# Kernel optimization log

Hardware: AMD Instinct MI355X
Metric: run time of the kernel (lower is better)

## Reference

```python
import jax, jax.numpy as jnp
import numpy as np

N = 50000
E = 800000
IN_DIM = 128
HID = 32
HEADS = 8
OUT_DIM = 64
BN_EPS = 1e-5
NEG_SLOPE = 0.2


def batch_norm(x, gamma, beta, mean, var):
    # eval-mode BatchNorm1d using running statistics
    return (x - mean) * jax.lax.rsqrt(var + BN_EPS) * gamma + beta


def gat_conv(x, src, dst, W, att_src, att_dst, heads, out_ch, n):
    """PyG GATConv (shared src/dst lin), self-loops already included in src/dst.
    x: [n, in]; W: [in, heads*out_ch]; att_*: [heads, out_ch].
    Returns [n, heads, out_ch]."""
    h = (x @ W).reshape(n, heads, out_ch)                       # node features per head
    a_s = jnp.einsum('nho,ho->nh', h, att_src)                  # [n, heads]
    a_d = jnp.einsum('nho,ho->nh', h, att_dst)
    e = jax.nn.leaky_relu(a_s[src] + a_d[dst], NEG_SLOPE)       # [e, heads]
    # segment softmax over incoming edges of each dst node
    mx = jax.ops.segment_max(e, dst, num_segments=n)
    ex = jnp.exp(e - mx[dst])
    denom = jax.ops.segment_sum(ex, dst, num_segments=n)
    alpha = ex / (denom[dst] + 1e-16)                           # [e, heads]
    out = jax.ops.segment_sum(alpha[:, :, None] * h[src], dst, num_segments=n)
    return out                                                  # [n, heads, out_ch]


def setup_inputs() -> dict:
    key = jax.random.key(0)
    ks = jax.random.split(key, 24)
    inp = {}
    inp['x'] = jax.random.normal(ks[0], (N, IN_DIM), dtype=jnp.float32)
    inp['edge_index'] = jax.random.randint(ks[1], (2, E), 0, N, dtype=jnp.int64)
    s = 0.05
    inp['W1'] = jax.random.normal(ks[2], (IN_DIM, HEADS * HID), dtype=jnp.float32) * s
    inp['a_src1'] = jax.random.normal(ks[3], (HEADS, HID), dtype=jnp.float32) * s
    inp['a_dst1'] = jax.random.normal(ks[4], (HEADS, HID), dtype=jnp.float32) * s
    inp['b1'] = jnp.zeros((HEADS * HID,), dtype=jnp.float32)
    inp['W2'] = jax.random.normal(ks[5], (HEADS * HID, OUT_DIM), dtype=jnp.float32) * s
    inp['a_src2'] = jax.random.normal(ks[6], (1, OUT_DIM), dtype=jnp.float32) * s
    inp['a_dst2'] = jax.random.normal(ks[7], (1, OUT_DIM), dtype=jnp.float32) * s
    inp['b2'] = jnp.zeros((OUT_DIM,), dtype=jnp.float32)
    # projection Linear(out_dim -> in_dim)
    inp['Wp'] = jax.random.normal(ks[8], (OUT_DIM, IN_DIM), dtype=jnp.float32) * s
    inp['bp'] = jnp.zeros((IN_DIM,), dtype=jnp.float32)
    # BatchNorm params (eval mode running stats)
    for i, d in [(1, HEADS * HID), (2, OUT_DIM), (3, IN_DIM)]:
        k0, k1, k2, k3 = jax.random.split(ks[8 + i], 4)
        inp[f'g{i}'] = 1.0 + 0.1 * jax.random.normal(k0, (d,), dtype=jnp.float32)
        inp[f'be{i}'] = 0.1 * jax.random.normal(k1, (d,), dtype=jnp.float32)
        inp[f'm{i}'] = 0.1 * jax.random.normal(k2, (d,), dtype=jnp.float32)
        inp[f'v{i}'] = jax.random.uniform(k3, (d,), dtype=jnp.float32, minval=0.5, maxval=1.5)
    return inp


def reference(x, edge_index, W1, a_src1, a_dst1, b1, W2, a_src2, a_dst2, b2,
              Wp, bp, g1, be1, m1, v1, g2, be2, m2, v2, g3, be3, m3, v3):
    n = x.shape[0]
    loops = jnp.arange(n, dtype=edge_index.dtype)
    src = jnp.concatenate([edge_index[0], loops])   # add_self_loops=True (PyG default)
    dst = jnp.concatenate([edge_index[1], loops])

    h = gat_conv(x, src, dst, W1, a_src1, a_dst1, HEADS, HID, n)
    h = h.reshape(n, HEADS * HID) + b1              # concat=True
    h = jax.nn.elu(batch_norm(h, g1, be1, m1, v1))  # dropout is no-op in eval

    h = gat_conv(h, src, dst, W2, a_src2, a_dst2, 1, OUT_DIM, n)
    h = h.reshape(n, OUT_DIM) + b2                  # concat=False, heads=1 -> mean == identity
    h = jax.nn.elu(batch_norm(h, g2, be2, m2, v2))

    h = h @ Wp + bp
    return batch_norm(h, g3, be3, m3, v3)
```

## Files before the change

### kernel.cpp

```cpp
#include <hip/hip_runtime.h>
#include <math.h>

#define NEG_SLOPE 0.2f
#define BN_EPS 1e-5f

typedef __bf16 bf16x8 __attribute__((ext_vector_type(8)));
typedef float  f32x4  __attribute__((ext_vector_type(4)));

__device__ __forceinline__ float elu_f(float x){ return x > 0.f ? x : expm1f(x); }
__device__ __forceinline__ float lrelu_f(float x){ return x > 0.f ? x : NEG_SLOPE * x; }

__device__ __forceinline__ float b2f(ushort u){
    union { uint i; float f; } v; v.i = (uint)u << 16; return v.f;
}
__device__ __forceinline__ ushort f2b(float f){
    union { float f; uint i; } v; v.f = f;
    uint r = v.i + 0x7FFFu + ((v.i >> 16) & 1u);
    return (ushort)(r >> 16);
}

__global__ void setup_kernel(const void* ei, int n_check, long long N, int* flag64,
    const float* __restrict__ W1, const float* __restrict__ W2, const float* __restrict__ Wp,
    ushort* __restrict__ wt1, ushort* __restrict__ wt2, ushort* __restrict__ wtp,
    const float* b1, const float* b2, const float* bp,
    const float* g1, const float* be1, const float* m1, const float* v1,
    const float* g2, const float* be2, const float* m2, const float* v2,
    const float* g3, const float* be3, const float* m3, const float* v3,
    float* par)
{
    int b = blockIdx.x, t = threadIdx.x;
    if (b == 0) {
        __shared__ int oks;
        if (t == 0) oks = 1;
        __syncthreads();
        const long long* p = (const long long*)ei;
        int ok = 1;
        for (int i = t; i < n_check; i += 256) {
            long long v = p[i];
            if (v < 0 || v >= N) ok = 0;
        }
        if (!ok) oks = 0;
        __syncthreads();
        if (t == 0) *flag64 = oks;
        { float s = g1[t] * rsqrtf(v1[t] + BN_EPS); par[t] = s;        par[256 + t] = b1[t] * s + be1[t] - m1[t] * s; }
        if (t < 64)  { float s = g2[t] * rsqrtf(v2[t] + BN_EPS); par[512 + t] = s;  par[576 + t] = b2[t] * s + be2[t] - m2[t] * s; }
        if (t < 128) { float s = g3[t] * rsqrtf(v3[t] + BN_EPS); par[640 + t] = s;  par[768 + t] = bp[t] * s + be3[t] - m3[t] * s; }
    } else {
        int idx = (b - 1) * 256 + t;
        if (idx < 32768) {
            int n = idx >> 7, k = idx & 127;
            wt1[idx] = f2b(W1[k * 256 + n]);
        } else if (idx < 49152) {
            int j = idx - 32768;
            int n = j >> 8, k = j & 255;
            wt2[j] = f2b(W2[k * 64 + n]);
        } else if (idx < 57344) {
            int j = idx - 49152;
            int n = j >> 6, k = j & 63;
            wtp[j] = f2b(Wp[k * 128 + n]);
        }
    }
}

__device__ __forceinline__ void get_edge(const void* ei, int e, int E, int f64, int& s, int& d)
{
    if (e < E) {
        if (f64) { const long long* p = (const long long*)ei; s = (int)p[e]; d = (int)p[E + e]; }
        else     { const int*       p = (const int*)ei;       s = p[e];      d = p[E + e]; }
    } else {
        s = d = e - E;
    }
}

__global__ void count_kernel(const void* ei, int E, int N, const int* flag64, int* deg)
{
    int i = blockIdx.x * blockDim.x + threadIdx.x;
    int ET = E + N;
    if (i >= ET) return;
    int s, d;
    get_edge(ei, i, E, *flag64, s, d);
    atomicAdd(&deg[d], 1);
}

__global__ void scan1_kernel(const int* __restrict__ deg, int N, int* __restrict__ bsum)
{
    int b = blockIdx.x, t = threadIdx.x;
    int base = b * 4096 + t * 16;
    int s = 0;
    #pragma unroll
    for (int k = 0; k < 16; k += 4) {
        int idx = base + k;
        if (idx + 3 < N) {
            int4 v = *reinterpret_cast<const int4*>(&deg[idx]);
            s += v.x + v.y + v.z + v.w;
        } else {
            for (int q = 0; q < 4; ++q) if (idx + q < N) s += deg[idx + q];
        }
    }
    #pragma unroll
    for (int off = 1; off < 64; off <<= 1) s += __shfl_xor(s, off);
    __shared__ int wsum[4];
    if ((t & 63) == 0) wsum[t >> 6] = s;
    __syncthreads();
    if (t == 0) bsum[b] = wsum[0] + wsum[1] + wsum[2] + wsum[3];
}

__global__ void scan2_kernel(const int* __restrict__ bsum, int nb, int* __restrict__ bpre)
{
    if (threadIdx.x == 0) {
        int r = 0;
        for (int i = 0; i < nb; ++i) { bpre[i] = r; r += bsum[i]; }
        bpre[nb] = r;
    }
}

__global__ void scan3_kernel(const int* __restrict__ deg, int N,
                             const int* __restrict__ bpre, int nb,
                             int* __restrict__ rowptr, int* __restrict__ fillptr)
{
    int b = blockIdx.x, t = threadIdx.x;
    int base = b * 4096 + t * 16;
    int loc[16];
    int s = 0;
    #pragma unroll
    for (int k = 0; k < 16; ++k) {
        int idx = base + k;
        int d = (idx < N) ? deg[idx] : 0;
        loc[k] = s; s += d;
    }
    int lane = t & 63;
    int incl = s;
    #pragma unroll
    for (int off = 1; off < 64; off <<= 1) {
        int v = __shfl_up(incl, off);
        if (lane >= off) incl += v;
    }
    __shared__ int wsum[4];
    if (lane == 63) wsum[t >> 6] = incl;
    __syncthreads();
    int woff = 0;
    int w = t >> 6;
    for (int i = 0; i < w; ++i) woff += wsum[i];
    int off0 = bpre[b] + woff + incl - s;
    #pragma unroll
    for (int k = 0; k < 16; ++k) {
        int idx = base + k;
        if (idx < N) { rowptr[idx] = off0 + loc[k]; fillptr[idx] = off0 + loc[k]; }
    }
    if (b == 0 && t == 0) rowptr[N] = bpre[nb];
}

__global__ void fill_kernel(const void* ei, int E, int N, const int* flag64,
                            int* fillptr, int* esrc)
{
    int i = blockIdx.x * blockDim.x + threadIdx.x;
    int ET = E + N;
    if (i >= ET) return;
    int s, d;
    get_edge(ei, i, E, *flag64, s, d);
    int pos = atomicAdd(&fillptr[d], 1);
    esrc[pos] = s;
}

template<int ATYPE, int OMODE>
__global__ __launch_bounds__(256) void mgemm_kernel(const void* __restrict__ Ap,
    const ushort* __restrict__ Bt, void* __restrict__ Cp, int M, int K, int NC,
    const float* __restrict__ S, const float* __restrict__ Cc)
{
    const int BM = 128, LDA = 72;
    __shared__ __align__(16) ushort As[BM][LDA];
    __shared__ __align__(16) ushort Bs[64][LDA];
    int t = threadIdx.x;
    int m0 = blockIdx.x * BM, n0 = blockIdx.y * 64;
    int w = t >> 6, l = t & 63;
    int wm = w >> 1, wn = w & 1;
    int r16 = l & 15, kg = l >> 4;

    f32x4 acc[4][2];
    #pragma unroll
    for (int mi = 0; mi < 4; ++mi)
        #pragma unroll
        for (int ni = 0; ni < 2; ++ni)
            acc[mi][ni] = (f32x4){0.f, 0.f, 0.f, 0.f};

    for (int kb = 0; kb < K; kb += 64) {
        if (ATYPE == 0) {
            const float* A = (const float*)Ap;
            #pragma unroll
            for (int p = 0; p < 8; ++p) {
                int r = (t >> 4) + p * 16, c4 = (t & 15) * 4;
                int gm = m0 + r;
                float4 v = (gm < M) ? *reinterpret_cast<const float4*>(&A[(size_t)gm * K + kb + c4])
                                    : make_float4(0.f, 0.f, 0.f, 0.f);
                ushort4 u; u.x = f2b(v.x); u.y = f2b(v.y); u.z = f2b(v.z); u.w = f2b(v.w);
                *reinterpret_cast<ushort4*>(&As[r][c4]) = u;
            }
        } else {
            const ushort* A = (const ushort*)Ap;
            #pragma unroll
            for (int p = 0; p < 4; ++p) {
                int r = (t >> 3) + p * 32, c8 = (t & 7) * 8;
                int gm = m0 + r;
                uint4 v = (gm < M) ? *reinterpret_cast<const uint4*>(&A[(size_t)gm * K + kb + c8])
                                   : make_uint4(0u, 0u, 0u, 0u);
                *reinterpret_cast<uint4*>(&As[r][c8]) = v;
            }
        }
        #pragma unroll
        for (int p = 0; p < 2; ++p) {
            int r = (t >> 3) + p * 32, c8 = (t & 7) * 8;
            uint4 v = *reinterpret_cast<const uint4*>(&Bt[(size_t)(n0 + r) * K + kb + c8]);
            *reinterpret_cast<uint4*>(&Bs[r][c8]) = v;
        }
        __syncthreads();
        #pragma unroll
        for (int kk = 0; kk < 2; ++kk) {
            bf16x8 bB[2], bA[4];
            #pragma unroll
            for (int ni = 0; ni < 2; ++ni)
                bB[ni] = *reinterpret_cast<const bf16x8*>(&Bs[wn * 32 + ni * 16 + r16][kk * 32 + kg * 8]);
            #pragma unroll
            for (int mi = 0; mi < 4; ++mi)
                bA[mi] = *reinterpret_cast<const bf16x8*>(&As[wm * 64 + mi * 16 + r16][kk * 32 + kg * 8]);
            #pragma unroll
            for (int mi = 0; mi < 4; ++mi)
                #pragma unroll
                for (int ni = 0; ni < 2; ++ni)
                    acc[mi][ni] = __builtin_amdgcn_mfma_f32_16x16x32_bf16(bA[mi], bB[ni], acc[mi][ni], 0, 0, 0);
        }
        __syncthreads();
    }
    #pragma unroll
    for (int mi = 0; mi < 4; ++mi) {
        #pragma unroll
        for (int ni = 0; ni < 2; ++ni) {
            #pragma unroll
            for (int rg = 0; rg < 4; ++rg) {
                int gm = m0 + wm * 64 + mi * 16 + kg * 4 + rg;
                int gc = n0 + wn * 32 + ni * 16 + r16;
                if (gm < M) {
                    float v = acc[mi][ni][rg];
                    if (OMODE == 0) ((ushort*)Cp)[(size_t)gm * NC + gc] = f2b(v);
                    else            ((float*)Cp)[(size_t)gm * NC + gc] = v * S[gc] + Cc[gc];
                }
            }
        }
    }
}

__global__ void att1_kernel(const ushort* __restrict__ h1,
                            const float* __restrict__ a_src, const float* __restrict__ a_dst,
                            float* __restrict__ as1, float* __restrict__ ad1, int N)
{
    int wid = (blockIdx.x * blockDim.x + threadIdx.x) >> 6;
    int lane = threadIdx.x & 63;
    if (wid >= N) return;
    ushort4 hv = *reinterpret_cast<const ushort4*>(&h1[(size_t)wid * 256 + lane * 4]);
    int f0 = lane * 4;
    float vx = b2f(hv.x), vy = b2f(hv.y), vz = b2f(hv.z), vw = b2f(hv.w);
    float s = vx * a_src[f0] + vy * a_src[f0 + 1] + vz * a_src[f0 + 2] + vw * a_src[f0 + 3];
    float d = vx * a_dst[f0] + vy * a_dst[f0 + 1] + vz * a_dst[f0 + 2] + vw * a_dst[f0 + 3];
    s += __shfl_xor(s, 1); s += __shfl_xor(s, 2); s += __shfl_xor(s, 4);
    d += __shfl_xor(d, 1); d += __shfl_xor(d, 2); d += __shfl_xor(d, 4);
    if ((lane & 7) == 0) {
        as1[wid * 8 + (lane >> 3)] = s;
        ad1[wid * 8 + (lane >> 3)] = d;
    }
}

__global__ void att2_kernel(const ushort* __restrict__ h2,
                            const float* __restrict__ a_src, const float* __restrict__ a_dst,
                            float* __restrict__ as2, float* __restrict__ ad2, int N)
{
    int wid = (blockIdx.x * blockDim.x + threadIdx.x) >> 6;
    int lane = threadIdx.x & 63;
    if (wid >= N) return;
    float v = b2f(h2[(size_t)wid * 64 + lane]);
    float s = v * a_src[lane];
    float d = v * a_dst[lane];
    #pragma unroll
    for (int off = 32; off; off >>= 1) {
        s += __shfl_down(s, off, 64);
        d += __shfl_down(d, off, 64);
    }
    if (lane == 0) { as2[wid] = s; ad2[wid] = d; }
}

__global__ void agg1_kernel(const ushort* __restrict__ h1,
                            const float* __restrict__ as1, const float* __restrict__ ad1,
                            const int* __restrict__ rowptr, const int* __restrict__ esrc,
                            const float* __restrict__ par,
                            ushort* __restrict__ outb, int N)
{
    int wid = (blockIdx.x * blockDim.x + threadIdx.x) >> 6;
    int lane = threadIdx.x & 63;
    if (wid >= N) return;
    int beg = rowptr[wid], end = rowptr[wid + 1];

    int h = lane & 7;
    float ad_h = ad1[wid * 8 + h];
    float den = 0.f;
    for (int i = beg + (lane >> 3); i < end; i += 8)
        den += __expf(lrelu_f(as1[esrc[i] * 8 + h] + ad_h));
    den += __shfl_xor(den, 8, 64);
    den += __shfl_xor(den, 16, 64);
    den += __shfl_xor(den, 32, 64);
    float inv = 1.f / (den + 1e-16f);

    int li = lane & 31, half = lane >> 5;
    int hh = li >> 2;
    float inv_h = __shfl(inv, hh, 64);
    float ad_hh = __shfl(ad_h, hh, 64);
    float acc[8] = {0.f, 0.f, 0.f, 0.f, 0.f, 0.f, 0.f, 0.f};

    auto edge1 = [&](int ii) {
        int src = esrc[ii];
        float al = __expf(lrelu_f(as1[src * 8 + hh] + ad_hh)) * inv_h;
        uint4 r = *reinterpret_cast<const uint4*>(&h1[(size_t)src * 256 + li * 8]);
        union { uint u; float f; } c0, c1;
        c0.u = r.x << 16; c1.u = r.x & 0xffff0000u; acc[0] += al * c0.f; acc[1] += al * c1.f;
        c0.u = r.y << 16; c1.u = r.y & 0xffff0000u; acc[2] += al * c0.f; acc[3] += al * c1.f;
        c0.u = r.z << 16; c1.u = r.z & 0xffff0000u; acc[4] += al * c0.f; acc[5] += al * c1.f;
        c0.u = r.w << 16; c1.u = r.w & 0xffff0000u; acc[6] += al * c0.f; acc[7] += al * c1.f;
    };
    int i = beg + half;
    for (; i + 2 < end; i += 4) { edge1(i); edge1(i + 2); }
    for (; i < end; i += 2) edge1(i);

    #pragma unroll
    for (int f = 0; f < 8; ++f) acc[f] += __shfl_xor(acc[f], 32, 64);
    if (half == 0) {
        int f0 = li * 8;
        const float* S1 = par;
        const float* C1 = par + 256;
        ushort o[8];
        #pragma unroll
        for (int f = 0; f < 8; ++f) o[f] = f2b(elu_f(acc[f] * S1[f0 + f] + C1[f0 + f]));
        uint4 pk;
        pk.x = (uint)o[0] | ((uint)o[1] << 16);
        pk.y = (uint)o[2] | ((uint)o[3] << 16);
        pk.z = (uint)o[4] | ((uint)o[5] << 16);
        pk.w = (uint)o[6] | ((uint)o[7] << 16);
        *reinterpret_cast<uint4*>(&outb[(size_t)wid * 256 + f0]) = pk;
    }
}

__global__ void agg2_kernel(const ushort* __restrict__ h2,
                            const float* __restrict__ as2, const float* __restrict__ ad2,
                            const int* __restrict__ rowptr, const int* __restrict__ esrc,
                            const float* __restrict__ par,
                            ushort* __restrict__ outb, int N)
{
    int wid = (blockIdx.x * blockDim.x + threadIdx.x) >> 6;
    int lane = threadIdx.x & 63;
    if (wid >= N) return;
    int beg = rowptr[wid], end = rowptr[wid + 1];
    float ad = ad2[wid];
    float den = 0.f;
    for (int i = beg + lane; i < end; i += 64)
        den += __expf(lrelu_f(as2[esrc[i]] + ad));
    #pragma unroll
    for (int off = 1; off < 64; off <<= 1) den += __shfl_xor(den, off, 64);
    float inv = 1.f / (den + 1e-16f);

    int li = lane & 31, half = lane >> 5;
    float a0 = 0.f, a1 = 0.f;
    auto edge1 = [&](int ii) {
        int src = esrc[ii];
        float al = __expf(lrelu_f(as2[src] + ad)) * inv;
        uint hv = *reinterpret_cast<const uint*>(&h2[(size_t)src * 64 + li * 2]);
        union { uint u; float f; } c0, c1;
        c0.u = hv << 16; c1.u = hv & 0xffff0000u;
        a0 += al * c0.f; a1 += al * c1.f;
    };
    int i = beg + half;
    for (; i + 2 < end; i += 4) { edge1(i); edge1(i + 2); }
    for (; i < end; i += 2) edge1(i);

    a0 += __shfl_xor(a0, 32, 64);
    a1 += __shfl_xor(a1, 32, 64);
    if (half == 0) {
        int f = li * 2;
        const float* S2 = par + 512;
        const float* C2 = par + 576;
        ushort2 o;
        o.x = f2b(elu_f(a0 * S2[f] + C2[f]));
        o.y = f2b(elu_f(a1 * S2[f + 1] + C2[f + 1]));
        *reinterpret_cast<ushort2*>(&outb[(size_t)wid * 64 + f]) = o;
    }
}

extern "C" void kernel_launch(void* const* d_in, const int* in_sizes, int n_in,
                              void* d_out, int out_size, void* d_ws, size_t ws_size,
                              hipStream_t stream)
{
    const float* x      = (const float*)d_in[0];
    const void*  ei     = d_in[1];
    const float* W1     = (const float*)d_in[2];
    const float* a_src1 = (const float*)d_in[3];
    const float* a_dst1 = (const float*)d_in[4];
    const float* b1     = (const float*)d_in[5];
    const float* W2     = (const float*)d_in[6];
    const float* a_src2 = (const float*)d_in[7];
    const float* a_dst2 = (const float*)d_in[8];
    const float* b2     = (const float*)d_in[9];
    const float* Wp     = (const float*)d_in[10];
    const float* bp     = (const float*)d_in[11];
    const float* g1 = (const float*)d_in[12], *be1 = (const float*)d_in[13];
    const float* m1 = (const float*)d_in[14], *v1  = (const float*)d_in[15];
    const float* g2 = (const float*)d_in[16], *be2 = (const float*)d_in[17];
    const float* m2 = (const float*)d_in[18], *v2  = (const float*)d_in[19];
    const float* g3 = (const float*)d_in[20], *be3 = (const float*)d_in[21];
    const float* m3 = (const float*)d_in[22], *v3  = (const float*)d_in[23];
    float* out = (float*)d_out;

    const int N  = in_sizes[0] / 128;
    const int E  = in_sizes[1] / 2;
    const int ET = E + N;

    char* base = (char*)d_ws;
    size_t off = 0;
    auto alloc = [&](size_t bytes) -> char* {
        char* p = base + off;
        off += (bytes + 255) & ~(size_t)255;
        return p;
    };
    float*  par     = (float*)alloc(1024 * 4);
    int*    flag64  = (int*)alloc(256);
    int*    bsum    = (int*)alloc(256);
    int*    bpre    = (int*)alloc(256);
    int*    rowptr  = (int*)alloc((size_t)(N + 1) * 4);
    int*    fillptr = (int*)alloc((size_t)(N + 1) * 4);
    int*    esrc    = (int*)alloc((size_t)ET * 4);
    float*  as1     = (float*)alloc((size_t)N * 8 * 4);
    float*  ad1     = (float*)alloc((size_t)N * 8 * 4);
    float*  as2     = (float*)alloc((size_t)N * 4);
    float*  ad2     = (float*)alloc((size_t)N * 4);
    ushort* wt1     = (ushort*)alloc(256 * 128 * 2);
    ushort* wt2     = (ushort*)alloc(64 * 256 * 2);
    ushort* wtp     = (ushort*)alloc(128 * 64 * 2);
    ushort* h1      = (ushort*)alloc((size_t)N * 256 * 2);
    ushort* h1b     = (ushort*)alloc((size_t)N * 256 * 2);
    ushort* h2      = (ushort*)alloc((size_t)N * 64 * 2);
    ushort* g2buf   = (ushort*)alloc((size_t)N * 64 * 2);

    setup_kernel<<<225, 256, 0, stream>>>(ei, min(2 * E, 4096), (long long)N, flag64,
        W1, W2, Wp, wt1, wt2, wtp,
        b1, b2, bp, g1, be1, m1, v1, g2, be2, m2, v2, g3, be3, m3, v3, par);
    hipMemsetAsync(fillptr, 0, (N + 1) * sizeof(int), stream);

    int ebl = (ET + 255) / 256;
    int nb = (N + 4095) / 4096;
    count_kernel<<<ebl, 256, 0, stream>>>(ei, E, N, flag64, fillptr);
    scan1_kernel<<<nb, 256, 0, stream>>>(fillptr, N, bsum);
    scan2_kernel<<<1, 64, 0, stream>>>(bsum, nb, bpre);
    scan3_kernel<<<nb, 256, 0, stream>>>(fillptr, N, bpre, nb, rowptr, fillptr);
    fill_kernel<<<ebl, 256, 0, stream>>>(ei, E, N, flag64, fillptr, esrc);

    int mb128 = (N + 127) / 128;
    int wbl   = (N + 3) / 4;
    mgemm_kernel<0, 0><<<dim3(mb128, 4), 256, 0, stream>>>(x, wt1, h1, N, 128, 256, nullptr, nullptr);
    att1_kernel<<<wbl, 256, 0, stream>>>(h1, a_src1, a_dst1, as1, ad1, N);
    agg1_kernel<<<wbl, 256, 0, stream>>>(h1, as1, ad1, rowptr, esrc, par, h1b, N);

    mgemm_kernel<1, 0><<<dim3(mb128, 1), 256, 0, stream>>>(h1b, wt2, h2, N, 256, 64, nullptr, nullptr);
    att2_kernel<<<wbl, 256, 0, stream>>>(h2, a_src2, a_dst2, as2, ad2, N);
    agg2_kernel<<<wbl, 256, 0, stream>>>(h2, as2, ad2, rowptr, esrc, par, g2buf, N);

    mgemm_kernel<1, 1><<<dim3(mb128, 2), 256, 0, stream>>>(g2buf, wtp, out, N, 64, 128, par + 640, par + 768);
}
```

Measured before the change: 313.2 us.

## Fuse layer-1 attention scores into GEMM epilogue and precompute normalized edge weights

The first GEMM now computes per-head source and destination attention logits in its epilogue through shuffle reductions, which removes the att1 pass that re-read h1. New wden kernels compute the exp weights and softmax denominators per edge and write normalized alphas to a per-edge buffer. The aggregation kernels then read those alphas instead of recomputing exp and gathering as[src], and their edge loop is unrolled 4x. The cost is extra global traffic: roughly 850K×8 floats are written and read back for layer 1, plus two more kernel launches.

```diff
diff --git a/kernel.cpp b/kernel.cpp
--- a/kernel.cpp
+++ b/kernel.cpp
@@ -162,10 +162,12 @@
     esrc[pos] = s;
 }
 
-template<int ATYPE, int OMODE>
+template<int ATYPE, int OMODE, int ATT>
 __global__ __launch_bounds__(256) void mgemm_kernel(const void* __restrict__ Ap,
     const ushort* __restrict__ Bt, void* __restrict__ Cp, int M, int K, int NC,
-    const float* __restrict__ S, const float* __restrict__ Cc)
+    const float* __restrict__ S, const float* __restrict__ Cc,
+    const float* __restrict__ att_s, const float* __restrict__ att_d,
+    float* __restrict__ as_out, float* __restrict__ ad_out)
 {
     const int BM = 128, LDA = 72;
     __shared__ __align__(16) ushort As[BM][LDA];
@@ -246,25 +248,39 @@
             }
         }
     }
-}
-
-__global__ void att1_kernel(const ushort* __restrict__ h1,
-                            const float* __restrict__ a_src, const float* __restrict__ a_dst,
-                            float* __restrict__ as1, float* __restrict__ ad1, int N)
-{
-    int wid = (blockIdx.x * blockDim.x + threadIdx.x) >> 6;
-    int lane = threadIdx.x & 63;
-    if (wid >= N) return;
-    ushort4 hv = *reinterpret_cast<const ushort4*>(&h1[(size_t)wid * 256 + lane * 4]);
-    int f0 = lane * 4;
-    float vx = b2f(hv.x), vy = b2f(hv.y), vz = b2f(hv.z), vw = b2f(hv.w);
-    float s = vx * a_src[f0] + vy * a_src[f0 + 1] + vz * a_src[f0 + 2] + vw * a_src[f0 + 3];
-    float d = vx * a_dst[f0] + vy * a_dst[f0 + 1] + vz * a_dst[f0 + 2] + vw * a_dst[f0 + 3];
-    s += __shfl_xor(s, 1); s += __shfl_xor(s, 2); s += __shfl_xor(s, 4);
-    d += __shfl_xor(d, 1); d += __shfl_xor(d, 2); d += __shfl_xor(d, 4);
-    if ((lane & 7) == 0) {
-        as1[wid * 8 + (lane >> 3)] = s;
-        ad1[wid * 8 + (lane >> 3)] = d;
+    if (ATT) {
+        int head = (n0 >> 5) + wn;
+        float cs0 = att_s[n0 + wn * 32 + r16], cs1 = att_s[n0 + wn * 32 + 16 + r16];
+        float cd0 = att_d[n0 + wn * 32 + r16], cd1 = att_d[n0 + wn * 32 + 16 + r16];
+        float sp[4][4], dp[4][4];
+        #pragma unroll
+        for (int mi = 0; mi < 4; ++mi)
+            #pragma unroll
+            for (int rg = 0; rg < 4; ++rg) {
+                sp[mi][rg] = acc[mi][0][rg] * cs0 + acc[mi][1][rg] * cs1;
+                dp[mi][rg] = acc[mi][0][rg] * cd0 + acc[mi][1][rg] * cd1;
+            }
+        #pragma unroll
+        for (int off = 1; off < 16; off <<= 1)
+            #pragma unroll
+            for (int mi = 0; mi < 4; ++mi)
+                #pragma unroll
+                for (int rg = 0; rg < 4; ++rg) {
+                    sp[mi][rg] += __shfl_xor(sp[mi][rg], off);
+                    dp[mi][rg] += __shfl_xor(dp[mi][rg], off);
+                }
+        if (r16 == 0) {
+            #pragma unroll
+            for (int mi = 0; mi < 4; ++mi)
+                #pragma unroll
+                for (int rg = 0; rg < 4; ++rg) {
+                    int gm = m0 + wm * 64 + mi * 16 + kg * 4 + rg;
+                    if (gm < M) {
+                        as_out[gm * 8 + head] = sp[mi][rg];
+                        ad_out[gm * 8 + head] = dp[mi][rg];
+                    }
+                }
+        }
     }
 }
 
@@ -286,8 +302,54 @@
     if (lane == 0) { as2[wid] = s; ad2[wid] = d; }
 }
 
-__global__ void agg1_kernel(const ushort* __restrict__ h1,
-                            const float* __restrict__ as1, const float* __restrict__ ad1,
+__global__ void wden1_kernel(const float* __restrict__ as1, const float* __restrict__ ad1,
+                             const int* __restrict__ rowptr, const int* __restrict__ esrc,
+                             float* __restrict__ walpha, int N)
+{
+    int wid = (blockIdx.x * blockDim.x + threadIdx.x) >> 6;
+    int lane = threadIdx.x & 63;
+    if (wid >= N) return;
+    int h = lane & 7, j = lane >> 3;
+    float ad = ad1[wid * 8 + h];
+    int beg = rowptr[wid], end = rowptr[wid + 1];
+    float den = 0.f;
+    for (int i = beg + j; i < end; i += 8) {
+        int src = esrc[i];
+        float w = __expf(lrelu_f(as1[src * 8 + h] + ad));
+        walpha[(size_t)i * 8 + h] = w;
+        den += w;
+    }
+    den += __shfl_xor(den, 8);
+    den += __shfl_xor(den, 16);
+    den += __shfl_xor(den, 32);
+    float inv = 1.f / (den + 1e-16f);
+    for (int i = beg + j; i < end; i += 8)
+        walpha[(size_t)i * 8 + h] *= inv;
+}
+
+__global__ void wden2_kernel(const float* __restrict__ as2, const float* __restrict__ ad2,
+                             const int* __restrict__ rowptr, const int* __restrict__ esrc,
+                             float* __restrict__ walpha, int N)
+{
+    int wid = (blockIdx.x * blockDim.x + threadIdx.x) >> 6;
+    int lane = threadIdx.x & 63;
+    if (wid >= N) return;
+    float ad = ad2[wid];
+    int beg = rowptr[wid], end = rowptr[wid + 1];
+    float den = 0.f;
+    for (int i = beg + lane; i < end; i += 64) {
+        float w = __expf(lrelu_f(as2[esrc[i]] + ad));
+        walpha[i] = w;
+        den += w;
+    }
+    #pragma unroll
+    for (int off = 1; off < 64; off <<= 1) den += __shfl_xor(den, off);
+    float inv = 1.f / (den + 1e-16f);
+    for (int i = beg + lane; i < end; i += 64)
+        walpha[i] *= inv;
+}
+
+__global__ void agg1_kernel(const ushort* __restrict__ h1, const float* __restrict__ walpha,
                             const int* __restrict__ rowptr, const int* __restrict__ esrc,
                             const float* __restrict__ par,
                             ushort* __restrict__ outb, int N)
@@ -296,26 +358,13 @@
     int lane = threadIdx.x & 63;
     if (wid >= N) return;
     int beg = rowptr[wid], end = rowptr[wid + 1];
-
-    int h = lane & 7;
-    float ad_h = ad1[wid * 8 + h];
-    float den = 0.f;
-    for (int i = beg + (lane >> 3); i < end; i += 8)
-        den += __expf(lrelu_f(as1[esrc[i] * 8 + h] + ad_h));
-    den += __shfl_xor(den, 8, 64);
-    den += __shfl_xor(den, 16, 64);
-    den += __shfl_xor(den, 32, 64);
-    float inv = 1.f / (den + 1e-16f);
-
     int li = lane & 31, half = lane >> 5;
     int hh = li >> 2;
-    float inv_h = __shfl(inv, hh, 64);
-    float ad_hh = __shfl(ad_h, hh, 64);
     float acc[8] = {0.f, 0.f, 0.f, 0.f, 0.f, 0.f, 0.f, 0.f};
 
     auto edge1 = [&](int ii) {
         int src = esrc[ii];
-        float al = __expf(lrelu_f(as1[src * 8 + hh] + ad_hh)) * inv_h;
+        float al = walpha[(size_t)ii * 8 + hh];
         uint4 r = *reinterpret_cast<const uint4*>(&h1[(size_t)src * 256 + li * 8]);
         union { uint u; float f; } c0, c1;
         c0.u = r.x << 16; c1.u = r.x & 0xffff0000u; acc[0] += al * c0.f; acc[1] += al * c1.f;
@@ -324,7 +373,7 @@
         c0.u = r.w << 16; c1.u = r.w & 0xffff0000u; acc[6] += al * c0.f; acc[7] += al * c1.f;
     };
     int i = beg + half;
-    for (; i + 2 < end; i += 4) { edge1(i); edge1(i + 2); }
+    for (; i + 6 < end; i += 8) { edge1(i); edge1(i + 2); edge1(i + 4); edge1(i + 6); }
     for (; i < end; i += 2) edge1(i);
 
     #pragma unroll
@@ -345,8 +394,7 @@
     }
 }
 
-__global__ void agg2_kernel(const ushort* __restrict__ h2,
-                            const float* __restrict__ as2, const float* __restrict__ ad2,
+__global__ void agg2_kernel(const ushort* __restrict__ h2, const float* __restrict__ walpha,
                             const int* __restrict__ rowptr, const int* __restrict__ esrc,
                             const float* __restrict__ par,
                             ushort* __restrict__ outb, int N)
@@ -355,26 +403,18 @@
     int lane = threadIdx.x & 63;
     if (wid >= N) return;
     int beg = rowptr[wid], end = rowptr[wid + 1];
-    float ad = ad2[wid];
-    float den = 0.f;
-    for (int i = beg + lane; i < end; i += 64)
-        den += __expf(lrelu_f(as2[esrc[i]] + ad));
-    #pragma unroll
-    for (int off = 1; off < 64; off <<= 1) den += __shfl_xor(den, off, 64);
-    float inv = 1.f / (den + 1e-16f);
-
     int li = lane & 31, half = lane >> 5;
     float a0 = 0.f, a1 = 0.f;
     auto edge1 = [&](int ii) {
         int src = esrc[ii];
-        float al = __expf(lrelu_f(as2[src] + ad)) * inv;
+        float al = walpha[ii];
         uint hv = *reinterpret_cast<const uint*>(&h2[(size_t)src * 64 + li * 2]);
         union { uint u; float f; } c0, c1;
         c0.u = hv << 16; c1.u = hv & 0xffff0000u;
         a0 += al * c0.f; a1 += al * c1.f;
     };
     int i = beg + half;
-    for (; i + 2 < end; i += 4) { edge1(i); edge1(i + 2); }
+    for (; i + 6 < end; i += 8) { edge1(i); edge1(i + 2); edge1(i + 4); edge1(i + 6); }
     for (; i < end; i += 2) edge1(i);
 
     a0 += __shfl_xor(a0, 32, 64);
@@ -439,6 +479,8 @@
     ushort* wt1     = (ushort*)alloc(256 * 128 * 2);
     ushort* wt2     = (ushort*)alloc(64 * 256 * 2);
     ushort* wtp     = (ushort*)alloc(128 * 64 * 2);
+    float*  walpha1 = (float*)alloc((size_t)ET * 8 * 4);
+    float*  walpha2 = (float*)alloc((size_t)ET * 4);
     ushort* h1      = (ushort*)alloc((size_t)N * 256 * 2);
     ushort* h1b     = (ushort*)alloc((size_t)N * 256 * 2);
     ushort* h2      = (ushort*)alloc((size_t)N * 64 * 2);
@@ -459,13 +501,17 @@
 
     int mb128 = (N + 127) / 128;
     int wbl   = (N + 3) / 4;
-    mgemm_kernel<0, 0><<<dim3(mb128, 4), 256, 0, stream>>>(x, wt1, h1, N, 128, 256, nullptr, nullptr);
-    att1_kernel<<<wbl, 256, 0, stream>>>(h1, a_src1, a_dst1, as1, ad1, N);
-    agg1_kernel<<<wbl, 256, 0, stream>>>(h1, as1, ad1, rowptr, esrc, par, h1b, N);
-
-    mgemm_kernel<1, 0><<<dim3(mb128, 1), 256, 0, stream>>>(h1b, wt2, h2, N, 256, 64, nullptr, nullptr);
+    mgemm_kernel<0, 0, 1><<<dim3(mb128, 4), 256, 0, stream>>>(x, wt1, h1, N, 128, 256,
+        nullptr, nullptr, a_src1, a_dst1, as1, ad1);
+    wden1_kernel<<<wbl, 256, 0, stream>>>(as1, ad1, rowptr, esrc, walpha1, N);
+    agg1_kernel<<<wbl, 256, 0, stream>>>(h1, walpha1, rowptr, esrc, par, h1b, N);
+
+    mgemm_kernel<1, 0, 0><<<dim3(mb128, 1), 256, 0, stream>>>(h1b, wt2, h2, N, 256, 64,
+        nullptr, nullptr, nullptr, nullptr, nullptr, nullptr);
     att2_kernel<<<wbl, 256, 0, stream>>>(h2, a_src2, a_dst2, as2, ad2, N);
-    agg2_kernel<<<wbl, 256, 0, stream>>>(h2, as2, ad2, rowptr, esrc, par, g2buf, N);
-
-    mgemm_kernel<1, 1><<<dim3(mb128, 2), 256, 0, stream>>>(g2buf, wtp, out, N, 64, 128, par + 640, par + 768);
-}
+    wden2_kernel<<<wbl, 256, 0, stream>>>(as2, ad2, rowptr, esrc, walpha2, N);
+    agg2_kernel<<<wbl, 256, 0, stream>>>(h2, walpha2, rowptr, esrc, par, g2buf, N);
+
+    mgemm_kernel<1, 1, 0><<<dim3(mb128, 2), 256, 0, stream>>>(g2buf, wtp, out, N, 64, 128,
+        par + 640, par + 768, nullptr, nullptr, nullptr, nullptr);
+}
```

After: 331.2 us. 5.8% more time.
